# Kernel tuning notes

Measured on AMD Instinct MI355X. Metric: run time of the kernel, lower is better.

Reference implementation:

```python
import jax, jax.numpy as jnp
import numpy as np

N, C_IN, C_OUT, P, W, H = 32, 32, 16, 4, 16, 16
D = P * P
EPS = 1e-6


def squash(s, axis=-1):
    # v = ||s||^2/(1+||s||^2) * s/||s||, eps-stabilized as in the repo (eps=1e-6)
    n2 = jnp.sum(s * s, axis=axis, keepdims=True)
    n = jnp.sqrt(n2)
    return (n2 / (1.0 + n2)) * s / (n + EPS)


def setup_inputs() -> dict:
    key = jax.random.key(0)
    k1, k2, k3 = jax.random.split(key, 3)
    l = jax.random.normal(k1, (N, C_IN, D, W, H), jnp.float32)
    g = jax.random.normal(k2, (N, C_OUT, D), jnp.float32)
    weight = jax.random.normal(k3, (1, C_IN, 1, C_OUT, P, P), jnp.float32)
    return {"l": l, "g": g, "weight": weight, "num_iters": 3}


def reference(l, g, weight, num_iters):
    n, c, d, w, h = l.shape
    p = weight.shape[-1]
    c_out = weight.shape[3]
    # (N, C, D, W, H) -> (N, C, W*H, P, P)
    lp = jnp.transpose(l, (0, 1, 3, 4, 2)).reshape(n, c, w * h, p, p)
    # votes: pose matmul against per-(in,out) transform matrices
    # v[n,c,s,o] = lp[n,c,s] @ weight[0,c,0,o]   -> (N, C, WH, C_out, P, P)
    v = jnp.einsum('ncsij,cojk->ncsoik', lp, weight[0, :, 0])
    M = c * w * h
    v = v.reshape(n, M, c_out, d)          # (N, M, C_out, D)
    g = g[:, None, :, :]                    # (N, 1, C_out, D)
    # dynamic routing, logits initialized from agreement with the prior global capsule g
    b = jnp.sum(v * g, axis=-1, keepdims=True)   # (N, M, C_out, 1)
    cc = None
    for _ in range(num_iters):
        cc = jax.nn.softmax(b, axis=1)           # attention over input votes M
        g = squash(jnp.sum(cc * v, axis=1, keepdims=True))  # (N, 1, C_out, D)
        b = b + jnp.sum(v * g, axis=-1, keepdims=True)
    a = jnp.squeeze(cc, -1)   # (N, M, C_out)
    g = jnp.squeeze(g, 1)     # (N, C_out, D)
    return a, g
```

## Files before the change

### kernel.cpp

```cpp
#include <hip/hip_runtime.h>
#include <math.h>

#define N_   32
#define CIN  32
#define COUT 16
#define D_   16
#define S_   256
#define M_   (CIN * S_)
#define NBLK (N_ * CIN)

#define LOG2E 1.4426950408889634f

#define PROW 20
#define PIDX(n, c, o) ((((size_t)(n) * CIN + (c)) * COUT + (o)) * PROW)

#define BSLOT 64

__device__ __forceinline__ float2 aload_f2(const float* p) {
  unsigned long long v = __hip_atomic_load(
      (const unsigned long long*)p, __ATOMIC_RELAXED, __HIP_MEMORY_SCOPE_AGENT);
  float2 r;
  r.x = __uint_as_float((unsigned)v);
  r.y = __uint_as_float((unsigned)(v >> 32));
  return r;
}
__device__ __forceinline__ void astore_f2(float* p, float a, float b) {
  unsigned long long v =
      ((unsigned long long)__float_as_uint(b) << 32) | __float_as_uint(a);
  __hip_atomic_store((unsigned long long*)p, v, __ATOMIC_RELAXED,
                     __HIP_MEMORY_SCOPE_AGENT);
}

#define SW(s) ((((s) & 3)) ^ (((s) >> 2) & 3))

__device__ __forceinline__ void stage_tile(const float* __restrict__ gsrc,
                                           float* ls, int tid) {
  const float4* src = (const float4*)gsrc;
#pragma unroll
  for (int j = 0; j < 4; j++) {
    int f = ((tid & 3) << 6) + (tid >> 2) + (j << 8);
    float4 val = src[f];
    int dd = f >> 6;
    int u  = f & 63;
    int chunk = dd >> 2, lo = dd & 3;
    float vv[4] = {val.x, val.y, val.z, val.w};
#pragma unroll
    for (int m = 0; m < 4; m++) {
      int s = (u << 2) + m;
      int p = chunk ^ SW(s);
      ls[(s << 4) + (p << 2) + lo] = vv[m];
    }
  }
}

__device__ __forceinline__ void read_lp(const float* ls, int s, float* lp) {
  const float4* row = (const float4*)(ls + (s << 4));
  int sw = SW(s);
#pragma unroll
  for (int c = 0; c < 4; c++) {
    float4 q = row[c ^ sw];
    lp[c * 4 + 0] = q.x; lp[c * 4 + 1] = q.y;
    lp[c * 4 + 2] = q.z; lp[c * 4 + 3] = q.w;
  }
}

__device__ __forceinline__ float dot16(const float* a, const float* b) {
  float a0 = 0.f, a1 = 0.f, a2 = 0.f, a3 = 0.f;
#pragma unroll
  for (int k = 0; k < 4; k++) {
    a0 = fmaf(a[k],      b[k],      a0);
    a1 = fmaf(a[4 + k],  b[4 + k],  a1);
    a2 = fmaf(a[8 + k],  b[8 + k],  a2);
    a3 = fmaf(a[12 + k], b[12 + k], a3);
  }
  return (a0 + a1) + (a2 + a3);
}

__device__ __forceinline__ void gbarrier(int* bar, int idx, int n, int tid) {
  __syncthreads();
  if (tid == 0) {
    int* base = bar + ((idx << 5) + n) * BSLOT;
    if (__hip_atomic_fetch_add(base, 1, __ATOMIC_RELAXED,
                               __HIP_MEMORY_SCOPE_AGENT) == CIN - 1) {
      __hip_atomic_store(base + 32, 1, __ATOMIC_RELAXED,
                         __HIP_MEMORY_SCOPE_AGENT);
    } else {
      int guard = 0;
      while (__hip_atomic_load(base + 32, __ATOMIC_RELAXED,
                               __HIP_MEMORY_SCOPE_AGENT) == 0) {
        __builtin_amdgcn_s_sleep(2);
        if (++guard > 5000000) break;
      }
    }
  }
  __syncthreads();
}

template <int PASS>
__device__ __forceinline__ void routing_pass(
    int n, int c, int tid, int o, int strip,
    const float* __restrict__ wgt,
    const float* __restrict__ part_in, float* __restrict__ part_out,
    const float* ls, float red[4][18][16], float red2[18][16],
    float hd[16][20], float* Gacc, float& shift) {
  if constexpr (PASS > 0) {
    if (tid < 64) {
      const int ho = tid & 15, hs = tid >> 4;
      float H[18];
#pragma unroll
      for (int f = 0; f < 17; f++) H[f] = 0.f;
      H[17] = -INFINITY;
#pragma unroll 2
      for (int q = 0; q < 8; q++) {
        const float* r = part_in + PIDX(n, hs + 4 * q, ho);
#pragma unroll
        for (int i = 0; i < 8; i++) {
          float2 v = aload_f2(r + 2 * i);
          H[2 * i + 0] += v.x;
          H[2 * i + 1] += v.y;
        }
        float2 t = aload_f2(r + 16);
        H[16] += t.x;
        H[17] = fmaxf(H[17], t.y);
      }
#pragma unroll
      for (int off = 16; off <= 32; off <<= 1) {
#pragma unroll
        for (int f = 0; f < 17; f++) H[f] += __shfl_xor(H[f], off);
        H[17] = fmaxf(H[17], __shfl_xor(H[17], off));
      }
      if (tid < 16) {
        float inv = 1.0f / H[16], n2 = 0.f, Sg[16];
#pragma unroll
        for (int d = 0; d < 16; d++) { Sg[d] = H[d] * inv; n2 = fmaf(Sg[d], Sg[d], n2); }
        float coef = n2 / ((1.f + n2) * (sqrtf(n2) + 1e-6f));
        float4* hq = (float4*)hd[tid];
#pragma unroll
        for (int i = 0; i < 4; i++)
          hq[i] = make_float4(coef * Sg[i * 4 + 0], coef * Sg[i * 4 + 1],
                              coef * Sg[i * 4 + 2], coef * Sg[i * 4 + 3]);
        hd[tid][16] = H[17];
      }
    }
    __syncthreads();
    const float4* hq = (const float4*)hd[o];
#pragma unroll
    for (int i = 0; i < 4; i++) {
      float4 v = hq[i];
      Gacc[i * 4 + 0] += v.x; Gacc[i * 4 + 1] += v.y;
      Gacc[i * 4 + 2] += v.z; Gacc[i * 4 + 3] += v.w;
    }
    shift = hd[o][16];
  }

  float WG[16];
  {
    float wreg[16];
    const float4* wp = (const float4*)(wgt + (c * COUT + o) * 16);
#pragma unroll
    for (int i = 0; i < 4; i++) {
      float4 t = wp[i];
      wreg[i * 4 + 0] = t.x; wreg[i * 4 + 1] = t.y;
      wreg[i * 4 + 2] = t.z; wreg[i * 4 + 3] = t.w;
    }
#pragma unroll
    for (int i = 0; i < 4; i++)
#pragma unroll
      for (int j = 0; j < 4; j++) {
        float acc = 0.f;
#pragma unroll
        for (int k = 0; k < 4; k++)
          acc = fmaf(wreg[j * 4 + k], Gacc[i * 4 + k], acc);
        WG[i * 4 + j] = acc * LOG2E;
      }
  }

  float se = 0.f, bmx = -INFINITY, E[16];
#pragma unroll
  for (int d = 0; d < 16; d++) E[d] = 0.f;

#pragma unroll 4
  for (int it = 0; it < 16; it++) {
    float lp[16];
    read_lp(ls, strip + (it << 4), lp);
    float b = dot16(lp, WG) - shift;
    float e = exp2f(b);
    bmx = fmaxf(bmx, b);
    se += e;
#pragma unroll
    for (int d = 0; d < 16; d++) E[d] = fmaf(e, lp[d], E[d]);
  }

#pragma unroll
  for (int off = 16; off <= 32; off <<= 1) {
    se += __shfl_xor(se, off);
    bmx = fmaxf(bmx, __shfl_xor(bmx, off));
#pragma unroll
    for (int d = 0; d < 16; d++) E[d] += __shfl_xor(E[d], off);
  }

  const int w = tid >> 6;
  if ((tid & 63) < 16) {
#pragma unroll
    for (int d = 0; d < 16; d++) red[w][d][o] = E[d];
    red[w][16][o] = se;
    red[w][17][o] = bmx;
  }
  __syncthreads();

  for (int p = tid; p < 288; p += 256) {
    int f = p >> 4, oo = p & 15;
    float v0 = red[0][f][oo], v1 = red[1][f][oo];
    float v2 = red[2][f][oo], v3 = red[3][f][oo];
    red2[f][oo] = (f == 17) ? fmaxf(fmaxf(v0, v1), fmaxf(v2, v3))
                            : ((v0 + v1) + (v2 + v3));
  }
  __syncthreads();

  if (tid < 16) {
    float wt[16];
    const float4* wp = (const float4*)(wgt + (c * COUT + tid) * 16);
#pragma unroll
    for (int i = 0; i < 4; i++) {
      float4 t = wp[i];
      wt[i * 4 + 0] = t.x; wt[i * 4 + 1] = t.y;
      wt[i * 4 + 2] = t.z; wt[i * 4 + 3] = t.w;
    }
    float Et[16];
#pragma unroll
    for (int d = 0; d < 16; d++) Et[d] = red2[d][tid];
    float* p0 = part_out + PIDX(n, c, tid);
#pragma unroll
    for (int i = 0; i < 4; i++) {
      float s0 = 0.f, s1 = 0.f, s2 = 0.f, s3 = 0.f;
#pragma unroll
      for (int j = 0; j < 4; j++) {
        s0 = fmaf(Et[i * 4 + j], wt[j * 4 + 0], s0);
        s1 = fmaf(Et[i * 4 + j], wt[j * 4 + 1], s1);
        s2 = fmaf(Et[i * 4 + j], wt[j * 4 + 2], s2);
        s3 = fmaf(Et[i * 4 + j], wt[j * 4 + 3], s3);
      }
      astore_f2(p0 + 4 * i + 0, s0, s1);
      astore_f2(p0 + 4 * i + 2, s2, s3);
    }
    astore_f2(p0 + 16, red2[16][tid], red2[17][tid] + shift);
  }
}

__global__ __launch_bounds__(256, 4) void fused_kernel(
    const float* __restrict__ l, const float* __restrict__ wgt,
    const float* __restrict__ g0, float* __restrict__ a_out,
    float* __restrict__ g_out, float* __restrict__ PB0,
    float* __restrict__ PB1, int* __restrict__ bar) {
  const int bid = blockIdx.x;
  const int n = bid >> 5;
  const int c = bid & 31;
  const int tid = threadIdx.x;
  const int o = tid & 15;
  const int strip = tid >> 4;

  __shared__ float ls[D_ * S_];
  __shared__ float red[4][18][16];
  __shared__ float red2[18][16];
  __shared__ float hd[16][20];
  __shared__ float sinv[16];

  stage_tile(l + ((size_t)(n * CIN + c)) * D_ * S_, ls, tid);

  float Gacc[16];
  {
    const float4* gp = (const float4*)(g0 + (n * COUT + o) * 16);
#pragma unroll
    for (int i = 0; i < 4; i++) {
      float4 u = gp[i];
      Gacc[i * 4 + 0] = u.x; Gacc[i * 4 + 1] = u.y;
      Gacc[i * 4 + 2] = u.z; Gacc[i * 4 + 3] = u.w;
    }
  }

  __syncthreads();

  float shift = 0.f;

  routing_pass<0>(n, c, tid, o, strip, wgt, nullptr, PB0, ls, red, red2, hd,
                  Gacc, shift);
  gbarrier(bar, 0, n, tid);
  routing_pass<1>(n, c, tid, o, strip, wgt, PB0, PB1, ls, red, red2, hd,
                  Gacc, shift);
  gbarrier(bar, 1, n, tid);
  routing_pass<2>(n, c, tid, o, strip, wgt, PB1, PB0, ls, red, red2, hd,
                  Gacc, shift);
  gbarrier(bar, 2, n, tid);

  if (tid < 16) {
    float se = 0.f;
    if (c == 0) {
      float Ssum[16];
#pragma unroll
      for (int d = 0; d < 16; d++) Ssum[d] = 0.f;
#pragma unroll 4
      for (int cc = 0; cc < CIN; cc++) {
        const float* r = PB0 + PIDX(n, cc, tid);
#pragma unroll
        for (int i = 0; i < 8; i++) {
          float2 v = aload_f2(r + 2 * i);
          Ssum[2 * i + 0] += v.x;
          Ssum[2 * i + 1] += v.y;
        }
        se += aload_f2(r + 16).x;
      }
      float inv = 1.0f / se, n2 = 0.f;
#pragma unroll
      for (int d = 0; d < 16; d++) { Ssum[d] *= inv; n2 = fmaf(Ssum[d], Ssum[d], n2); }
      float coef = n2 / ((1.f + n2) * (sqrtf(n2) + 1e-6f));
      float* go = g_out + (n * COUT + tid) * 16;
#pragma unroll
      for (int d = 0; d < 16; d++) go[d] = coef * Ssum[d];
      sinv[tid] = inv;
    } else {
#pragma unroll 8
      for (int cc = 0; cc < CIN; cc++)
        se += aload_f2(PB0 + PIDX(n, cc, tid) + 16).x;
      sinv[tid] = 1.0f / se;
    }
  }
  __syncthreads();

  float WG[16];
  {
    float wreg[16];
    const float4* wp = (const float4*)(wgt + (c * COUT + o) * 16);
#pragma unroll
    for (int i = 0; i < 4; i++) {
      float4 t = wp[i];
      wreg[i * 4 + 0] = t.x; wreg[i * 4 + 1] = t.y;
      wreg[i * 4 + 2] = t.z; wreg[i * 4 + 3] = t.w;
    }
#pragma unroll
    for (int i = 0; i < 4; i++)
#pragma unroll
      for (int j = 0; j < 4; j++) {
        float acc = 0.f;
#pragma unroll
        for (int k = 0; k < 4; k++)
          acc = fmaf(wreg[j * 4 + k], Gacc[i * 4 + k], acc);
        WG[i * 4 + j] = acc * LOG2E;
      }
  }
  const float myinv = sinv[o];
  float* abase = a_out + ((size_t)(n * M_ + c * S_)) * COUT;
#pragma unroll 4
  for (int it = 0; it < 16; it++) {
    float lp[16];
    read_lp(ls, strip + (it << 4), lp);
    float b = dot16(lp, WG) - shift;
    abase[(size_t)((strip + (it << 4)) * COUT + o)] = exp2f(b) * myinv;
  }
}

extern "C" void kernel_launch(void* const* d_in, const int* in_sizes, int n_in,
                              void* d_out, int out_size, void* d_ws, size_t ws_size,
                              hipStream_t stream) {
  const float* l = (const float*)d_in[0];
  const float* g = (const float*)d_in[1];
  const float* w = (const float*)d_in[2];

  float* out = (float*)d_out;
  float* a_out = out;
  float* g_out = out + (size_t)N_ * M_ * COUT;

  float* ws = (float*)d_ws;
  float* PB0 = ws;
  float* PB1 = ws + (size_t)N_ * CIN * COUT * PROW;
  int* bar = (int*)(ws + 2 * (size_t)N_ * CIN * COUT * PROW);

  hipMemsetAsync(bar, 0, 3 * N_ * BSLOT * sizeof(int), stream);

  fused_kernel<<<NBLK, 256, 0, stream>>>(l, w, g, a_out, g_out, PB0, PB1, bar);
}
```

Before: 124.2 us.

## Replace per-block partial buffers with atomic accumulators and fuse final output pass

Each block now atomically adds its per-output-capsule partial sums into one shared accumulator per sample instead of writing separate partials that every block must re-reduce after the barrier. The running max shift is replaced with a log2 of the previous softmax denominator. The final pass writes unnormalised exponentials during the last routing iteration and rescales them in place with vectorised loads, avoiding a recompute of the logits. This trades redundant cross-block reads for contended float atomics and non-deterministic summation order, and adds a read-modify-write over the output.

```diff
diff --git a/kernel.cpp b/kernel.cpp
--- a/kernel.cpp
+++ b/kernel.cpp
@@ -11,10 +11,14 @@
 
 #define LOG2E 1.4426950408889634f
 
-#define PROW 20
-#define PIDX(n, c, o) ((((size_t)(n) * CIN + (c)) * COUT + (o)) * PROW)
+#define AROW 18
+#define AIDX(n, o) ((((size_t)(n) * COUT) + (o)) * AROW)
 
 #define BSLOT 64
+
+#define WS_ACC0 6144
+#define WS_ACC1 (6144 + 9216)
+#define WS_ACC2 (6144 + 2 * 9216)
 
 __device__ __forceinline__ float2 aload_f2(const float* p) {
   unsigned long long v = __hip_atomic_load(
@@ -24,11 +28,9 @@
   r.y = __uint_as_float((unsigned)(v >> 32));
   return r;
 }
-__device__ __forceinline__ void astore_f2(float* p, float a, float b) {
-  unsigned long long v =
-      ((unsigned long long)__float_as_uint(b) << 32) | __float_as_uint(a);
-  __hip_atomic_store((unsigned long long*)p, v, __ATOMIC_RELAXED,
-                     __HIP_MEMORY_SCOPE_AGENT);
+__device__ __forceinline__ void afadd(float* p, float v) {
+  (void)__hip_atomic_fetch_add(p, v, __ATOMIC_RELAXED,
+                               __HIP_MEMORY_SCOPE_AGENT);
 }
 
 #define SW(s) ((((s) & 3)) ^ (((s) >> 2) & 3))
@@ -100,47 +102,31 @@
 __device__ __forceinline__ void routing_pass(
     int n, int c, int tid, int o, int strip,
     const float* __restrict__ wgt,
-    const float* __restrict__ part_in, float* __restrict__ part_out,
-    const float* ls, float red[4][18][16], float red2[18][16],
+    const float* __restrict__ acc_in, float* __restrict__ acc_out,
+    float* __restrict__ a_out,
+    const float* ls, float red[4][17][16], float red2[17][16],
     float hd[16][20], float* Gacc, float& shift) {
   if constexpr (PASS > 0) {
-    if (tid < 64) {
-      const int ho = tid & 15, hs = tid >> 4;
-      float H[18];
-#pragma unroll
-      for (int f = 0; f < 17; f++) H[f] = 0.f;
-      H[17] = -INFINITY;
-#pragma unroll 2
-      for (int q = 0; q < 8; q++) {
-        const float* r = part_in + PIDX(n, hs + 4 * q, ho);
-#pragma unroll
-        for (int i = 0; i < 8; i++) {
-          float2 v = aload_f2(r + 2 * i);
-          H[2 * i + 0] += v.x;
-          H[2 * i + 1] += v.y;
-        }
-        float2 t = aload_f2(r + 16);
-        H[16] += t.x;
-        H[17] = fmaxf(H[17], t.y);
-      }
-#pragma unroll
-      for (int off = 16; off <= 32; off <<= 1) {
-#pragma unroll
-        for (int f = 0; f < 17; f++) H[f] += __shfl_xor(H[f], off);
-        H[17] = fmaxf(H[17], __shfl_xor(H[17], off));
-      }
-      if (tid < 16) {
-        float inv = 1.0f / H[16], n2 = 0.f, Sg[16];
-#pragma unroll
-        for (int d = 0; d < 16; d++) { Sg[d] = H[d] * inv; n2 = fmaf(Sg[d], Sg[d], n2); }
-        float coef = n2 / ((1.f + n2) * (sqrtf(n2) + 1e-6f));
-        float4* hq = (float4*)hd[tid];
-#pragma unroll
-        for (int i = 0; i < 4; i++)
-          hq[i] = make_float4(coef * Sg[i * 4 + 0], coef * Sg[i * 4 + 1],
-                              coef * Sg[i * 4 + 2], coef * Sg[i * 4 + 3]);
-        hd[tid][16] = H[17];
-      }
+    if (tid < 16) {
+      const float* r = acc_in + AIDX(n, tid);
+      float H[16];
+#pragma unroll
+      for (int i = 0; i < 8; i++) {
+        float2 v = aload_f2(r + 2 * i);
+        H[2 * i + 0] = v.x;
+        H[2 * i + 1] = v.y;
+      }
+      float se = aload_f2(r + 16).x;
+      float inv = 1.0f / se, n2 = 0.f, Sg[16];
+#pragma unroll
+      for (int d = 0; d < 16; d++) { Sg[d] = H[d] * inv; n2 = fmaf(Sg[d], Sg[d], n2); }
+      float coef = n2 / ((1.f + n2) * (sqrtf(n2) + 1e-6f));
+      float4* hq = (float4*)hd[tid];
+#pragma unroll
+      for (int i = 0; i < 4; i++)
+        hq[i] = make_float4(coef * Sg[i * 4 + 0], coef * Sg[i * 4 + 1],
+                            coef * Sg[i * 4 + 2], coef * Sg[i * 4 + 3]);
+      hd[tid][16] = __log2f(se);
     }
     __syncthreads();
     const float4* hq = (const float4*)hd[o];
@@ -150,7 +136,7 @@
       Gacc[i * 4 + 0] += v.x; Gacc[i * 4 + 1] += v.y;
       Gacc[i * 4 + 2] += v.z; Gacc[i * 4 + 3] += v.w;
     }
-    shift = hd[o][16];
+    shift += hd[o][16];
   }
 
   float WG[16];
@@ -175,9 +161,11 @@
       }
   }
 
-  float se = 0.f, bmx = -INFINITY, E[16];
+  float se = 0.f, E[16];
 #pragma unroll
   for (int d = 0; d < 16; d++) E[d] = 0.f;
+
+  float* abase = a_out + ((size_t)(n * M_ + c * S_)) * COUT;
 
 #pragma unroll 4
   for (int it = 0; it < 16; it++) {
@@ -185,7 +173,9 @@
     read_lp(ls, strip + (it << 4), lp);
     float b = dot16(lp, WG) - shift;
     float e = exp2f(b);
-    bmx = fmaxf(bmx, b);
+    if constexpr (PASS == 2) {
+      abase[(size_t)((strip + (it << 4)) * COUT + o)] = e;
+    }
     se += e;
 #pragma unroll
     for (int d = 0; d < 16; d++) E[d] = fmaf(e, lp[d], E[d]);
@@ -194,7 +184,6 @@
 #pragma unroll
   for (int off = 16; off <= 32; off <<= 1) {
     se += __shfl_xor(se, off);
-    bmx = fmaxf(bmx, __shfl_xor(bmx, off));
 #pragma unroll
     for (int d = 0; d < 16; d++) E[d] += __shfl_xor(E[d], off);
   }
@@ -204,16 +193,13 @@
 #pragma unroll
     for (int d = 0; d < 16; d++) red[w][d][o] = E[d];
     red[w][16][o] = se;
-    red[w][17][o] = bmx;
-  }
-  __syncthreads();
-
-  for (int p = tid; p < 288; p += 256) {
+  }
+  __syncthreads();
+
+  for (int p = tid; p < 272; p += 256) {
     int f = p >> 4, oo = p & 15;
-    float v0 = red[0][f][oo], v1 = red[1][f][oo];
-    float v2 = red[2][f][oo], v3 = red[3][f][oo];
-    red2[f][oo] = (f == 17) ? fmaxf(fmaxf(v0, v1), fmaxf(v2, v3))
-                            : ((v0 + v1) + (v2 + v3));
+    red2[f][oo] = ((red[0][f][oo] + red[1][f][oo]) +
+                   (red[2][f][oo] + red[3][f][oo]));
   }
   __syncthreads();
 
@@ -229,7 +215,7 @@
     float Et[16];
 #pragma unroll
     for (int d = 0; d < 16; d++) Et[d] = red2[d][tid];
-    float* p0 = part_out + PIDX(n, c, tid);
+    float* pa = acc_out + AIDX(n, tid);
 #pragma unroll
     for (int i = 0; i < 4; i++) {
       float s0 = 0.f, s1 = 0.f, s2 = 0.f, s3 = 0.f;
@@ -240,18 +226,19 @@
         s2 = fmaf(Et[i * 4 + j], wt[j * 4 + 2], s2);
         s3 = fmaf(Et[i * 4 + j], wt[j * 4 + 3], s3);
       }
-      astore_f2(p0 + 4 * i + 0, s0, s1);
-      astore_f2(p0 + 4 * i + 2, s2, s3);
-    }
-    astore_f2(p0 + 16, red2[16][tid], red2[17][tid] + shift);
+      afadd(pa + 4 * i + 0, s0); afadd(pa + 4 * i + 1, s1);
+      afadd(pa + 4 * i + 2, s2); afadd(pa + 4 * i + 3, s3);
+    }
+    afadd(pa + 16, red2[16][tid]);
   }
 }
 
 __global__ __launch_bounds__(256, 4) void fused_kernel(
     const float* __restrict__ l, const float* __restrict__ wgt,
     const float* __restrict__ g0, float* __restrict__ a_out,
-    float* __restrict__ g_out, float* __restrict__ PB0,
-    float* __restrict__ PB1, int* __restrict__ bar) {
+    float* __restrict__ g_out, float* __restrict__ acc0,
+    float* __restrict__ acc1, float* __restrict__ acc2,
+    int* __restrict__ bar) {
   const int bid = blockIdx.x;
   const int n = bid >> 5;
   const int c = bid & 31;
@@ -260,8 +247,8 @@
   const int strip = tid >> 4;
 
   __shared__ float ls[D_ * S_];
-  __shared__ float red[4][18][16];
-  __shared__ float red2[18][16];
+  __shared__ float red[4][17][16];
+  __shared__ float red2[17][16];
   __shared__ float hd[16][20];
   __shared__ float sinv[16];
 
@@ -282,79 +269,51 @@
 
   float shift = 0.f;
 
-  routing_pass<0>(n, c, tid, o, strip, wgt, nullptr, PB0, ls, red, red2, hd,
-                  Gacc, shift);
+  routing_pass<0>(n, c, tid, o, strip, wgt, nullptr, acc0, a_out, ls, red,
+                  red2, hd, Gacc, shift);
   gbarrier(bar, 0, n, tid);
-  routing_pass<1>(n, c, tid, o, strip, wgt, PB0, PB1, ls, red, red2, hd,
-                  Gacc, shift);
+  routing_pass<1>(n, c, tid, o, strip, wgt, acc0, acc1, a_out, ls, red,
+                  red2, hd, Gacc, shift);
   gbarrier(bar, 1, n, tid);
-  routing_pass<2>(n, c, tid, o, strip, wgt, PB1, PB0, ls, red, red2, hd,
-                  Gacc, shift);
+  routing_pass<2>(n, c, tid, o, strip, wgt, acc1, acc2, a_out, ls, red,
+                  red2, hd, Gacc, shift);
   gbarrier(bar, 2, n, tid);
 
   if (tid < 16) {
-    float se = 0.f;
+    const float* r = acc2 + AIDX(n, tid);
+    float se = aload_f2(r + 16).x;
+    float inv = 1.0f / se;
+    sinv[tid] = inv;
     if (c == 0) {
-      float Ssum[16];
-#pragma unroll
-      for (int d = 0; d < 16; d++) Ssum[d] = 0.f;
-#pragma unroll 4
-      for (int cc = 0; cc < CIN; cc++) {
-        const float* r = PB0 + PIDX(n, cc, tid);
-#pragma unroll
-        for (int i = 0; i < 8; i++) {
-          float2 v = aload_f2(r + 2 * i);
-          Ssum[2 * i + 0] += v.x;
-          Ssum[2 * i + 1] += v.y;
-        }
-        se += aload_f2(r + 16).x;
-      }
-      float inv = 1.0f / se, n2 = 0.f;
-#pragma unroll
-      for (int d = 0; d < 16; d++) { Ssum[d] *= inv; n2 = fmaf(Ssum[d], Ssum[d], n2); }
+      float Sv[16];
+#pragma unroll
+      for (int i = 0; i < 8; i++) {
+        float2 v = aload_f2(r + 2 * i);
+        Sv[2 * i + 0] = v.x;
+        Sv[2 * i + 1] = v.y;
+      }
+      float n2 = 0.f;
+#pragma unroll
+      for (int d = 0; d < 16; d++) { Sv[d] *= inv; n2 = fmaf(Sv[d], Sv[d], n2); }
       float coef = n2 / ((1.f + n2) * (sqrtf(n2) + 1e-6f));
       float* go = g_out + (n * COUT + tid) * 16;
 #pragma unroll
-      for (int d = 0; d < 16; d++) go[d] = coef * Ssum[d];
-      sinv[tid] = inv;
-    } else {
-#pragma unroll 8
-      for (int cc = 0; cc < CIN; cc++)
-        se += aload_f2(PB0 + PIDX(n, cc, tid) + 16).x;
-      sinv[tid] = 1.0f / se;
-    }
-  }
-  __syncthreads();
-
-  float WG[16];
-  {
-    float wreg[16];
-    const float4* wp = (const float4*)(wgt + (c * COUT + o) * 16);
-#pragma unroll
-    for (int i = 0; i < 4; i++) {
-      float4 t = wp[i];
-      wreg[i * 4 + 0] = t.x; wreg[i * 4 + 1] = t.y;
-      wreg[i * 4 + 2] = t.z; wreg[i * 4 + 3] = t.w;
-    }
-#pragma unroll
-    for (int i = 0; i < 4; i++)
-#pragma unroll
-      for (int j = 0; j < 4; j++) {
-        float acc = 0.f;
-#pragma unroll
-        for (int k = 0; k < 4; k++)
-          acc = fmaf(wreg[j * 4 + k], Gacc[i * 4 + k], acc);
-        WG[i * 4 + j] = acc * LOG2E;
-      }
-  }
-  const float myinv = sinv[o];
-  float* abase = a_out + ((size_t)(n * M_ + c * S_)) * COUT;
-#pragma unroll 4
-  for (int it = 0; it < 16; it++) {
-    float lp[16];
-    read_lp(ls, strip + (it << 4), lp);
-    float b = dot16(lp, WG) - shift;
-    abase[(size_t)((strip + (it << 4)) * COUT + o)] = exp2f(b) * myinv;
+      for (int d = 0; d < 16; d++) go[d] = coef * Sv[d];
+    }
+  }
+  __syncthreads();
+
+  float4* pv = (float4*)(a_out + ((size_t)(n * M_ + c * S_)) * COUT);
+#pragma unroll
+  for (int r = 0; r < 4; r++) {
+    int i4 = tid + (r << 8);
+    int o0 = (i4 & 3) << 2;
+    float4 v = pv[i4];
+    v.x *= sinv[o0 + 0];
+    v.y *= sinv[o0 + 1];
+    v.z *= sinv[o0 + 2];
+    v.w *= sinv[o0 + 3];
+    pv[i4] = v;
   }
 }
 
@@ -370,11 +329,13 @@
   float* g_out = out + (size_t)N_ * M_ * COUT;
 
   float* ws = (float*)d_ws;
-  float* PB0 = ws;
-  float* PB1 = ws + (size_t)N_ * CIN * COUT * PROW;
-  int* bar = (int*)(ws + 2 * (size_t)N_ * CIN * COUT * PROW);
-
-  hipMemsetAsync(bar, 0, 3 * N_ * BSLOT * sizeof(int), stream);
-
-  fused_kernel<<<NBLK, 256, 0, stream>>>(l, w, g, a_out, g_out, PB0, PB1, bar);
-}
+  int* bar = (int*)ws;
+  float* acc0 = ws + WS_ACC0;
+  float* acc1 = ws + WS_ACC1;
+  float* acc2 = ws + WS_ACC2;
+
+  hipMemsetAsync(ws, 0, 135168, stream);
+
+  fused_kernel<<<NBLK, 256, 0, stream>>>(l, w, g, a_out, g_out, acc0, acc1,
+                                         acc2, bar);
+}
```

New measurement: 171.3 us. 1.38x slower.
